# Performance work log

Measured on AMD Instinct MI355X. Metric: run time of the kernel, lower is better.

The kernel has to match this reference:

```python
import jax, jax.numpy as jnp
import numpy as np

N_NODES = 50000


def gcn_conv(x, src, dst, W, b, n_nodes):
    # PyG GCNConv: add self-loops, symmetric normalization D^-1/2 (A+I) D^-1/2 (x W) + b
    E = src.shape[0]
    deg = jax.ops.segment_sum(jnp.ones((E,), x.dtype), dst, num_segments=n_nodes) + 1.0
    dinv = jax.lax.rsqrt(deg)
    h = x @ W  # [N, H]
    norm = dinv[src] * dinv[dst]  # [E]
    agg = jax.ops.segment_sum(h[src] * norm[:, None], dst, num_segments=n_nodes)
    agg = agg + h * (dinv * dinv)[:, None]  # self-loop contribution
    return agg + b


def setup_inputs() -> dict:
    key = jax.random.key(0)
    ks = jax.random.split(key, 16)
    N, E, D, H, T, O = N_NODES, 800000, 128, 128, 2, 1
    x = jax.random.normal(ks[0], (N, D), jnp.float32)
    edge_index = jax.random.randint(ks[1], (2, E), 0, N, jnp.int32)
    edge_attrs = jax.random.uniform(ks[2], (T, E, 7), jnp.float32)
    s = lambda k, sh: jax.random.normal(k, sh, jnp.float32) * (1.0 / np.sqrt(sh[0]))
    return {
        "x": x, "edge_index": edge_index, "edge_attrs": edge_attrs,
        "W1": s(ks[3], (D, H)), "b1": jnp.zeros((H,), jnp.float32),
        "W2": s(ks[4], (H, H)), "b2": jnp.zeros((H,), jnp.float32),
        "W3": s(ks[5], (H, H)), "b3": jnp.zeros((H,), jnp.float32),
        "We": s(ks[6], (2 * H + 7, H)), "be": jnp.zeros((H,), jnp.float32),
        "Wg": s(ks[7], (H, O)), "bg": jnp.zeros((O,), jnp.float32),
    }


def reference(x, edge_index, edge_attrs, W1, b1, W2, b2, W3, b3, We, be, Wg, bg):
    src, dst = edge_index[0], edge_index[1]
    n = x.shape[0]
    outputs = []
    for t in range(edge_attrs.shape[0]):  # small fixed T, x evolves across iterations
        edge_attr = edge_attrs[t]
        x = jax.nn.relu(gcn_conv(x, src, dst, W1, b1, n))
        x = jax.nn.relu(gcn_conv(x, src, dst, W2, b2, n))
        x = jax.nn.relu(gcn_conv(x, src, dst, W3, b3, n))
        # gather-concat-MLP-mean per edge
        edge_features = jnp.concatenate([x[src], x[dst], edge_attr], axis=1)
        edge_output = jax.nn.relu(edge_features @ We + be)
        graph_features = jnp.mean(edge_output, axis=0, keepdims=True)  # [1, H]
        outputs.append(graph_features @ Wg + bg)
        W1 = W2  # no-op placeholder removed below
        W1 = W1  # keep W1 unchanged
    return jnp.concatenate(outputs, axis=0)  # [T, output_dim]
```

## Files before the change

### kernel.cpp

```cpp
#include <hip/hip_runtime.h>
#include <hip/hip_bf16.h>


typedef __attribute__((ext_vector_type(8))) short bf16x8;
typedef __attribute__((ext_vector_type(4))) float f32x4;
typedef __attribute__((ext_vector_type(2))) float f32x2;

__device__ __forceinline__ unsigned short f2bf(float f) {
    union { float f; unsigned int u; } v; v.f = f;
    unsigned int r = v.u + 0x7fffu + ((v.u >> 16) & 1u);
    return (unsigned short)(r >> 16);
}
__device__ __forceinline__ unsigned int pk2bf(float lo, float hi) {
    return (unsigned int)f2bf(lo) | ((unsigned int)f2bf(hi) << 16);
}
__device__ __forceinline__ unsigned char f2fp8(float f) {
    return (unsigned char)(__builtin_amdgcn_cvt_pk_fp8_f32(f, f, 0, false) & 0xff);
}
__device__ __forceinline__ f32x2 max0_2(f32x2 v) {
#if __has_builtin(__builtin_elementwise_max)
    return __builtin_elementwise_max(v, (f32x2){0.f, 0.f});
#else
    return (f32x2){fmaxf(v[0], 0.f), fmaxf(v[1], 0.f)};
#endif
}

__global__ void to_bf16(const float* __restrict__ in, unsigned short* __restrict__ out, int n4)
{
    int i = blockIdx.x * 256 + threadIdx.x;
    if (i < n4) {
        float4 v = ((const float4*)in)[i];
        ushort4 o;
        o.x = f2bf(v.x); o.y = f2bf(v.y); o.z = f2bf(v.z); o.w = f2bf(v.w);
        ((ushort4*)out)[i] = o;
    }
}

__global__ void transpose_w(
    const float* __restrict__ W1, const float* __restrict__ W2,
    const float* __restrict__ W3, const float* __restrict__ We,
    unsigned short* __restrict__ T1, unsigned short* __restrict__ T2,
    unsigned short* __restrict__ T3, unsigned short* __restrict__ Tuv)
{
    const float* src; unsigned short* dst;
    switch (blockIdx.y) {
        case 0:  src = W1;             dst = T1;               break;
        case 1:  src = W2;             dst = T2;               break;
        case 2:  src = W3;             dst = T3;               break;
        case 3:  src = We;             dst = Tuv;              break;
        case 4:  src = We + 128 * 128; dst = Tuv + 128 * 128;  break;
        default: src = W2;             dst = Tuv + 256 * 128;  break;
    }
    for (int i = blockIdx.x * 256 + threadIdx.x; i < 128 * 128; i += 256 * gridDim.x) {
        int k = i >> 7, c = i & 127;
        dst[c * 128 + k] = f2bf(src[i]);
    }
}

__global__ __launch_bounds__(256) void mfma_matmul(
    const unsigned short* __restrict__ X, const unsigned short* __restrict__ Wt,
    unsigned char* __restrict__ out, const float* __restrict__ scale, int n_rows)
{
    const int wave = threadIdx.x >> 6;
    const int lane = threadIdx.x & 63;
    const int m = lane & 15;
    const int q = lane >> 4;
    const int r = blockIdx.x * 64 + wave * 16 + m;
    const bool rv = r < n_rows;

    f32x4 acc[8];
    #pragma unroll
    for (int i = 0; i < 8; ++i) acc[i] = (f32x4){0.f, 0.f, 0.f, 0.f};

    #pragma unroll
    for (int k0 = 0; k0 < 128; k0 += 32) {
        bf16x8 a = {};
        if (rv) a = *(const bf16x8*)(X + (size_t)r * 128 + k0 + q * 8);
        #pragma unroll
        for (int ct = 0; ct < 8; ++ct) {
            bf16x8 b = *(const bf16x8*)(Wt + (ct * 16 + m) * 128 + k0 + q * 8);
            acc[ct] = __builtin_amdgcn_mfma_f32_16x16x32_bf16(a, b, acc[ct], 0, 0, 0);
        }
    }

    #pragma unroll
    for (int reg = 0; reg < 4; ++reg) {
        int gr = blockIdx.x * 64 + wave * 16 + q * 4 + reg;
        if (gr >= n_rows) continue;
        float s = scale[gr];
        #pragma unroll
        for (int ct = 0; ct < 8; ++ct)
            out[(size_t)gr * 128 + ct * 16 + m] = f2fp8(acc[ct][reg] * s);
    }
}

#define FPAD 136
#define GN 16
#define ICAP 64
#define ISTR 72
#define FUSED_LDS (GN * FPAD * 2 + GN * ISTR * 4)
#define EM_CHUNK 512
#define EDGE_LDS (EM_CHUNK * 7 * 4 + EM_CHUNK * 4 * 2 + 512 * 4)

__device__ __forceinline__ void fused_body(
    int bx, char* smem,
    const unsigned char* __restrict__ hs_in, const int* __restrict__ csr_src,
    const int* __restrict__ offs, const int* __restrict__ counts,
    const float* __restrict__ dinv, const float* __restrict__ bias,
    const unsigned short* __restrict__ Wt, int ncols, int uvcols,
    unsigned char* __restrict__ buv, unsigned char* __restrict__ bh, int n)
{
    unsigned short* xs = (unsigned short*)smem;
    int* idxl = (int*)(smem + GN * FPAD * 2);
    const int tid = threadIdx.x;
    const int row = tid >> 5;
    const int node = bx * GN + row;
    const int lg = tid & 31;
    const int c4 = lg * 4;

    if (node < n) {
        const int off = offs[node];
        const int cnt = counts[node];
        const int cap = min(cnt, ICAP);

        for (int j = lg; j < cap; j += 32)
            idxl[row * ISTR + j] = csr_src[off + j];

        const unsigned int sv = *(const unsigned int*)(hs_in + (size_t)node * 128 + c4);

        f32x2 a01 = {0.f, 0.f}, a23 = {0.f, 0.f};
        auto de4 = [&](unsigned int v) {
            a01 += __builtin_amdgcn_cvt_pk_f32_fp8(v, false);
            a23 += __builtin_amdgcn_cvt_pk_f32_fp8(v, true);
        };
        unsigned int A[4], B[4];
        auto LQ = [&](unsigned int* Q, int jb) {
            #pragma unroll
            for (int q = 0; q < 4; ++q)
                Q[q] = *(const unsigned int*)(hs_in + (size_t)idxl[row * ISTR + jb + q] * 128 + c4);
        };
        auto CONS = [&](unsigned int* Q) {
            #pragma unroll
            for (int q = 0; q < 4; ++q) de4(Q[q]);
        };

        int j = 0;
        if (cap >= 8) {
            LQ(A, 0); LQ(B, 4);
            de4(sv);
            j = 8;
            for (; j + 8 <= cap; j += 8) {
                CONS(A); LQ(A, j);
                CONS(B); LQ(B, j + 4);
            }
            CONS(A); CONS(B);
        } else if (cap >= 4) {
            LQ(A, 0);
            de4(sv);
            CONS(A);
            j = 4;
        } else {
            de4(sv);
        }
        if (j + 4 <= cap) {
            LQ(A, j); CONS(A); j += 4;
        }
        for (; j < cap; ++j)
            de4(*(const unsigned int*)(hs_in + (size_t)idxl[row * ISTR + j] * 128 + c4));
        for (; j < cnt; ++j)
            de4(*(const unsigned int*)(hs_in + (size_t)csr_src[off + j] * 128 + c4));

        const float dn = dinv[node];
        const float4 bb = *(const float4*)(bias + c4);
        float r0 = fmaxf(fmaf(a01[0], dn, bb.x), 0.f);
        float r1 = fmaxf(fmaf(a01[1], dn, bb.y), 0.f);
        float r2 = fmaxf(fmaf(a23[0], dn, bb.z), 0.f);
        float r3 = fmaxf(fmaf(a23[1], dn, bb.w), 0.f);
        uint2 w;
        w.x = pk2bf(r0, r1); w.y = pk2bf(r2, r3);
        *(uint2*)&xs[row * FPAD + c4] = w;
    }
    __syncthreads();

    const int wave = tid >> 6;
    const int lane = tid & 63;
    const int m = lane & 15;
    const int q = lane >> 4;
    const int nct = ncols >> 4;
    const int per = nct >> 3;
    const int ct0 = wave * per;

    for (int ci = 0; ci < per; ++ci) {
        const int ct = ct0 + ci;
        f32x4 acc = (f32x4){0.f, 0.f, 0.f, 0.f};
        #pragma unroll
        for (int k0 = 0; k0 < 128; k0 += 32) {
            bf16x8 a = *(const bf16x8*)&xs[m * FPAD + k0 + q * 8];
            bf16x8 b = *(const bf16x8*)(Wt + (size_t)(ct * 16 + m) * 128 + k0 + q * 8);
            acc = __builtin_amdgcn_mfma_f32_16x16x32_bf16(a, b, acc, 0, 0, 0);
        }
        const int col = ct * 16 + m;
        #pragma unroll
        for (int reg = 0; reg < 4; ++reg) {
            int nd = bx * GN + q * 4 + reg;
            if (nd >= n) continue;
            if (col < uvcols)
                buv[(size_t)nd * 256 + col] = f2fp8(acc[reg]);
            else
                bh[(size_t)nd * 128 + col - uvcols] = f2fp8(acc[reg] * dinv[nd]);
        }
    }
}

__device__ __forceinline__ void edge_body(
    int chunk, char* smem,
    const unsigned char* __restrict__ uv, const int* __restrict__ src,
    const int* __restrict__ dst, const float* __restrict__ ea,
    const float* __restrict__ We_e, const float* __restrict__ be,
    const float* __restrict__ Wg, float* __restrict__ acc, int E)
{
    float* eas = (float*)smem;
    int*   ss  = (int*)(smem + EM_CHUNK * 7 * 4);
    int*   ds  = (int*)(smem + EM_CHUNK * 7 * 4 + EM_CHUNK * 4);
    float* red = (float*)(smem + EM_CHUNK * 7 * 4 + EM_CHUNK * 8);

    const int tid  = threadIdx.x;
    const int lane = tid & 31;
    const int g    = tid >> 5;
    const int c4   = lane * 4;

    f32x2 wlo[7], whi[7];
    #pragma unroll
    for (int i = 0; i < 7; ++i) {
        float4 wv = *(const float4*)(We_e + i * 128 + c4);
        wlo[i] = (f32x2){wv.x, wv.y};
        whi[i] = (f32x2){wv.z, wv.w};
    }
    const float4 bev = *(const float4*)(be + c4);
    const f32x2 be01 = (f32x2){bev.x, bev.y};
    const f32x2 be23 = (f32x2){bev.z, bev.w};
    const float4 wg4 = *(const float4*)(Wg + c4);

    f32x2 part01 = {0.f, 0.f}, part23 = {0.f, 0.f};

    const int base = chunk * EM_CHUNK;
    const int nch = min(EM_CHUNK, E - base);
    for (int i = tid; i < nch * 7; i += 512)
        eas[i] = ea[(size_t)base * 7 + i];
    for (int i = tid; i < nch; i += 512) {
        ss[i] = src[base + i];
        ds[i] = dst[base + i];
    }
    __syncthreads();

    auto ev = [&](int j) {
        unsigned int us = *(const unsigned int*)(uv + (size_t)ss[j] * 256 + c4);
        unsigned int vs = *(const unsigned int*)(uv + (size_t)ds[j] * 256 + 128 + c4);
        f32x2 u01 = __builtin_amdgcn_cvt_pk_f32_fp8(us, false);
        f32x2 u23 = __builtin_amdgcn_cvt_pk_f32_fp8(us, true);
        f32x2 v01 = __builtin_amdgcn_cvt_pk_f32_fp8(vs, false);
        f32x2 v23 = __builtin_amdgcn_cvt_pk_f32_fp8(vs, true);
        f32x2 val01 = u01 + v01 + be01;
        f32x2 val23 = u23 + v23 + be23;
        const float* eav = &eas[j * 7];
        #pragma unroll
        for (int i = 0; i < 7; ++i) {
            f32x2 e2 = (f32x2){eav[i], eav[i]};
            val01 += e2 * wlo[i];
            val23 += e2 * whi[i];
        }
        part01 += max0_2(val01);
        part23 += max0_2(val23);
    };

    int j = g;
    for (; j + 64 <= nch; j += 64) {
        ev(j); ev(j + 16); ev(j + 32); ev(j + 48);
    }
    for (; j < nch; j += 16)
        ev(j);
    __syncthreads();

    float p = part01[0] * wg4.x + part01[1] * wg4.y + part23[0] * wg4.z + part23[1] * wg4.w;
    red[tid] = p;
    __syncthreads();
    for (int s = 256; s > 0; s >>= 1) {
        if (tid < s) red[tid] += red[tid + s];
        __syncthreads();
    }
    if (tid == 0) atomicAdd(acc, red[0]);
}

__global__ __launch_bounds__(512, 8) void fused_gm(
    const unsigned char* __restrict__ hs_in, const int* __restrict__ csr_src,
    const int* __restrict__ offs, const int* __restrict__ counts,
    const float* __restrict__ dinv, const float* __restrict__ bias,
    const unsigned short* __restrict__ Wt, int ncols, int uvcols,
    unsigned char* __restrict__ buv, unsigned char* __restrict__ bh, int n)
{
    __shared__ __align__(16) char smem[FUSED_LDS];
    fused_body(blockIdx.x, smem, hs_in, csr_src, offs, counts, dinv, bias,
               Wt, ncols, uvcols, buv, bh, n);
}

__global__ __launch_bounds__(512, 8) void edge_mlp(
    const unsigned char* __restrict__ uv, const int* __restrict__ src,
    const int* __restrict__ dst, const float* __restrict__ ea,
    const float* __restrict__ We_e, const float* __restrict__ be,
    const float* __restrict__ Wg, float* __restrict__ acc, int E)
{
    __shared__ __align__(16) char smem[EDGE_LDS];
    edge_body(blockIdx.x, smem, uv, src, dst, ea, We_e, be, Wg, acc, E);
}

__global__ __launch_bounds__(512, 8) void fused_gm_edge(
    int nf,
    const unsigned char* __restrict__ hs_in, const int* __restrict__ csr_src,
    const int* __restrict__ offs, const int* __restrict__ counts,
    const float* __restrict__ dinv, const float* __restrict__ bias,
    const unsigned short* __restrict__ Wt, int ncols, int uvcols,
    unsigned char* __restrict__ buv, unsigned char* __restrict__ bh, int n,
    int ne, int ec0,
    const unsigned char* __restrict__ uv, const int* __restrict__ src,
    const int* __restrict__ dst, const float* __restrict__ ea,
    const float* __restrict__ We_e, const float* __restrict__ be,
    const float* __restrict__ Wg, float* __restrict__ acc, int E)
{
    __shared__ __align__(16) char smem[EDGE_LDS];
    const int bid = blockIdx.x;
    const int nmin = (nf < ne) ? nf : ne;
    const int nch8 = nmin >> 3;
    const int inter = nch8 * 16;
    int role, idx;
    if (bid < inter) {
        int gg = bid >> 4, s = bid & 15;
        role = s >> 3;
        idx = gg * 8 + (s & 7);
    } else {
        int r = bid - inter;
        int fleft = nf - nch8 * 8;
        if (r < fleft) { role = 0; idx = nch8 * 8 + r; }
        else           { role = 1; idx = nch8 * 8 + (r - fleft); }
    }
    if (role == 0)
        fused_body(idx, smem, hs_in, csr_src, offs, counts, dinv, bias,
                   Wt, ncols, uvcols, buv, bh, n);
    else
        edge_body(ec0 + idx, smem, uv, src, dst, ea, We_e, be, Wg, acc, E);
}

__global__ void count_edges(const int* __restrict__ dst, int* __restrict__ counts,
                            int* __restrict__ rank, int E)
{
    int e = blockIdx.x * 256 + threadIdx.x;
    if (e < E) rank[e] = atomicAdd(&counts[dst[e]], 1);
}

__global__ void scan1(const int* __restrict__ counts, int* __restrict__ scanned,
                      int* __restrict__ btot, float* __restrict__ dinv, int n)
{
    __shared__ int sh[256];
    int i = blockIdx.x * 256 + threadIdx.x;
    int v = (i < n) ? counts[i] : 0;
    if (i < n) dinv[i] = rsqrtf((float)v + 1.0f);
    sh[threadIdx.x] = v;
    __syncthreads();
    for (int off = 1; off < 256; off <<= 1) {
        int t = (threadIdx.x >= off) ? sh[threadIdx.x - off] : 0;
        __syncthreads();
        sh[threadIdx.x] += t;
        __syncthreads();
    }
    if (i < n) scanned[i] = sh[threadIdx.x] - v;
    if (threadIdx.x == 255) btot[blockIdx.x] = sh[255];
}

__global__ void scan2(int* __restrict__ btot, int nb)
{
    __shared__ int sh[256];
    int v = (threadIdx.x < nb) ? btot[threadIdx.x] : 0;
    sh[threadIdx.x] = v;
    __syncthreads();
    for (int off = 1; off < 256; off <<= 1) {
        int t = (threadIdx.x >= off) ? sh[threadIdx.x - off] : 0;
        __syncthreads();
        sh[threadIdx.x] += t;
        __syncthreads();
    }
    if (threadIdx.x < nb) btot[threadIdx.x] = sh[threadIdx.x] - v;
}

__global__ void scan3(const int* __restrict__ scanned, const int* __restrict__ btot,
                      int* __restrict__ offs, int n)
{
    int i = blockIdx.x * 256 + threadIdx.x;
    if (i < n) offs[i] = scanned[i] + btot[blockIdx.x];
}

__global__ void fill_csr2(const int* __restrict__ src, const int* __restrict__ dst,
                          const int* __restrict__ rank, const int* __restrict__ offs,
                          int* __restrict__ csr_src, int E, int n)
{
    const int g8 = blockIdx.x & 7;
    const int b8 = blockIdx.x >> 3;
    const int nb8 = gridDim.x >> 3;
    const int chunk = (n + 7) >> 3;
    const int lo = g8 * chunk;
    const int hi = min(n, lo + chunk);
    for (int e = b8 * 256 + threadIdx.x; e < E; e += nb8 * 256) {
        int d = dst[e];
        if (d >= lo && d < hi)
            csr_src[offs[d] + rank[e]] = src[e];
    }
}

__global__ void write_out(const float* __restrict__ acc, const float* __restrict__ bg,
                          float* __restrict__ out, float invE, int T)
{
    int t = threadIdx.x;
    if (t < T) out[t] = acc[t] * invE + bg[0];
}


extern "C" void kernel_launch(void* const* d_in, const int* in_sizes, int n_in,
                              void* d_out, int out_size, void* d_ws, size_t ws_size,
                              hipStream_t stream)
{
    const float* x   = (const float*)d_in[0];
    const int*  eidx = (const int*)d_in[1];
    const float* ea  = (const float*)d_in[2];
    const float* W1  = (const float*)d_in[3];
    const float* b1  = (const float*)d_in[4];
    const float* W2  = (const float*)d_in[5];
    const float* b2  = (const float*)d_in[6];
    const float* W3  = (const float*)d_in[7];
    const float* b3  = (const float*)d_in[8];
    const float* We  = (const float*)d_in[9];
    const float* be  = (const float*)d_in[10];
    const float* Wg  = (const float*)d_in[11];
    const float* bg  = (const float*)d_in[12];

    const int N = in_sizes[0] / 128;
    const int E = in_sizes[1] / 2;
    const int T = in_sizes[2] / (E * 7);
    const int* src = eidx;
    const int* dst = eidx + E;

    char* wsp = (char*)d_ws;
    auto alloc = [&](size_t bytes) -> char* {
        char* p = wsp;
        wsp += (bytes + 255) / 256 * 256;
        return p;
    };
    int*   counts  = (int*)alloc((size_t)N * 4);
    int*   offs    = (int*)alloc((size_t)N * 4);
    int*   scanned = (int*)alloc((size_t)N * 4);
    int*   btot    = (int*)alloc(1024);
    int*   rank    = (int*)alloc((size_t)E * 4);
    int*   csr_src = (int*)alloc((size_t)E * 4);
    float* dinv    = (float*)alloc((size_t)N * 4);
    float* acc     = (float*)alloc(256);
    unsigned short* X0  = (unsigned short*)alloc((size_t)N * 128 * 2);
    unsigned char*  Bh0 = (unsigned char*)alloc((size_t)N * 128);
    unsigned char*  Bh1 = (unsigned char*)alloc((size_t)N * 128);
    unsigned char*  Buv = (unsigned char*)alloc((size_t)N * 256);
    unsigned short* T1  = (unsigned short*)alloc(128 * 128 * 2);
    unsigned short* T2  = (unsigned short*)alloc(128 * 128 * 2);
    unsigned short* T3  = (unsigned short*)alloc(128 * 128 * 2);
    unsigned short* Tuv = (unsigned short*)alloc(384 * 128 * 2);

    hipMemsetAsync(counts, 0, (size_t)N * 4, stream);
    hipMemsetAsync(acc, 0, (size_t)T * 4, stream);

    to_bf16<<<(N * 128 / 4 + 255) / 256, 256, 0, stream>>>(x, X0, N * 128 / 4);
    transpose_w<<<dim3(8, 6), 256, 0, stream>>>(W1, W2, W3, We, T1, T2, T3, Tuv);

    count_edges<<<(E + 255) / 256, 256, 0, stream>>>(dst, counts, rank, E);
    const int nb = (N + 255) / 256;
    scan1<<<nb, 256, 0, stream>>>(counts, scanned, btot, dinv, N);
    scan2<<<1, 256, 0, stream>>>(btot, nb);
    scan3<<<nb, 256, 0, stream>>>(scanned, btot, offs, N);
    fill_csr2<<<2048, 256, 0, stream>>>(src, dst, rank, offs, csr_src, E, N);

    const int mmb = (N + 63) / 64;
    const int fgb = (N + GN - 1) / GN;
    const int emb = (E + EM_CHUNK - 1) / EM_CHUNK;
    const int eh0 = (emb + 1) / 2;
    const int eh1 = emb - eh0;

    unsigned char* hcur = Bh0;
    unsigned char* hnxt = Bh1;
    auto swap = [&]() { unsigned char* tmp = hcur; hcur = hnxt; hnxt = tmp; };

    mfma_matmul<<<mmb, 256, 0, stream>>>(X0, T1, hcur, dinv, N);
    fused_gm<<<fgb, 512, 0, stream>>>(hcur, csr_src, offs, counts, dinv, b1,
                                      T2, 128, 0, Buv, hnxt, N);
    swap();
    fused_gm<<<fgb, 512, 0, stream>>>(hcur, csr_src, offs, counts, dinv, b2,
                                      T3, 128, 0, Buv, hnxt, N);
    swap();

    for (int t = 0; t < T; ++t) {
        const bool last = (t == T - 1);
        fused_gm<<<fgb, 512, 0, stream>>>(hcur, csr_src, offs, counts, dinv, b3,
                                          Tuv, last ? 256 : 384, 256, Buv, hnxt, N);
        if (last) {
            edge_mlp<<<emb, 512, 0, stream>>>(Buv, src, dst, ea + (size_t)t * E * 7,
                                              We + 256 * 128, be, Wg, acc + t, E);
        } else {
            swap();
            fused_gm_edge<<<fgb + eh0, 512, 0, stream>>>(
                fgb, hcur, csr_src, offs, counts, dinv, b1, T2, 128, 0, Buv, hnxt, N,
                eh0, 0, Buv, src, dst, ea + (size_t)t * E * 7,
                We + 256 * 128, be, Wg, acc + t, E);
            swap();
            fused_gm_edge<<<fgb + eh1, 512, 0, stream>>>(
                fgb, hcur, csr_src, offs, counts, dinv, b2, T3, 128, 0, Buv, hnxt, N,
                eh1, eh0, Buv, src, dst, ea + (size_t)t * E * 7,
                We + 256 * 128, be, Wg, acc + t, E);
            swap();
        }
    }
    write_out<<<1, 64, 0, stream>>>(acc, bg, (float*)d_out, 1.0f / (float)E, T);
}
```

Baseline: 563.0 us.

## Split fused gather+matmul into separate gather and column-tiled matmul kernels

Splits the fused aggregation+MFMA kernel into a gather/ReLU kernel that writes bf16 activations to global memory and a separate matmul kernel that tiles 64 rows by 128 columns, using a grid y dimension for the uv/h column groups. Block size drops to 256 threads and the edge-MLP chunk to 256 edges. The edge kernel now loops over chunks, and all edge work overlaps with only the first gather of the next timestep instead of being split across two launches. The aim is to drop the per-block sync and the small 16-row MFMA tiles that reload weights for every block. The cost is extra global traffic for the intermediate activations and more kernel launches.

```diff
diff --git a/kernel.cpp b/kernel.cpp
--- a/kernel.cpp
+++ b/kernel.cpp
@@ -94,135 +94,154 @@
     }
 }
 
-#define FPAD 136
-#define GN 16
+#define GNODES 8
 #define ICAP 64
 #define ISTR 72
-#define FUSED_LDS (GN * FPAD * 2 + GN * ISTR * 4)
-#define EM_CHUNK 512
-#define EDGE_LDS (EM_CHUNK * 7 * 4 + EM_CHUNK * 4 * 2 + 512 * 4)
-
-__device__ __forceinline__ void fused_body(
-    int bx, char* smem,
+#define GATHER_LDS (GNODES * ISTR * 4)
+#define EM_CHUNK 256
+#define EDGE_LDS 10240
+
+__device__ __forceinline__ void gather_body(
+    int bx, int* idxl,
     const unsigned char* __restrict__ hs_in, const int* __restrict__ csr_src,
     const int* __restrict__ offs, const int* __restrict__ counts,
     const float* __restrict__ dinv, const float* __restrict__ bias,
-    const unsigned short* __restrict__ Wt, int ncols, int uvcols,
-    unsigned char* __restrict__ buv, unsigned char* __restrict__ bh, int n)
-{
-    unsigned short* xs = (unsigned short*)smem;
-    int* idxl = (int*)(smem + GN * FPAD * 2);
+    unsigned short* __restrict__ xout, int n)
+{
     const int tid = threadIdx.x;
     const int row = tid >> 5;
-    const int node = bx * GN + row;
+    const int node = bx * GNODES + row;
     const int lg = tid & 31;
     const int c4 = lg * 4;
 
-    if (node < n) {
-        const int off = offs[node];
-        const int cnt = counts[node];
-        const int cap = min(cnt, ICAP);
-
-        for (int j = lg; j < cap; j += 32)
-            idxl[row * ISTR + j] = csr_src[off + j];
-
-        const unsigned int sv = *(const unsigned int*)(hs_in + (size_t)node * 128 + c4);
-
-        f32x2 a01 = {0.f, 0.f}, a23 = {0.f, 0.f};
-        auto de4 = [&](unsigned int v) {
-            a01 += __builtin_amdgcn_cvt_pk_f32_fp8(v, false);
-            a23 += __builtin_amdgcn_cvt_pk_f32_fp8(v, true);
-        };
-        unsigned int A[4], B[4];
-        auto LQ = [&](unsigned int* Q, int jb) {
-            #pragma unroll
-            for (int q = 0; q < 4; ++q)
-                Q[q] = *(const unsigned int*)(hs_in + (size_t)idxl[row * ISTR + jb + q] * 128 + c4);
-        };
-        auto CONS = [&](unsigned int* Q) {
-            #pragma unroll
-            for (int q = 0; q < 4; ++q) de4(Q[q]);
-        };
-
-        int j = 0;
-        if (cap >= 8) {
-            LQ(A, 0); LQ(B, 4);
-            de4(sv);
-            j = 8;
-            for (; j + 8 <= cap; j += 8) {
-                CONS(A); LQ(A, j);
-                CONS(B); LQ(B, j + 4);
-            }
-            CONS(A); CONS(B);
-        } else if (cap >= 4) {
-            LQ(A, 0);
-            de4(sv);
-            CONS(A);
-            j = 4;
-        } else {
-            de4(sv);
-        }
-        if (j + 4 <= cap) {
-            LQ(A, j); CONS(A); j += 4;
-        }
-        for (; j < cap; ++j)
-            de4(*(const unsigned int*)(hs_in + (size_t)idxl[row * ISTR + j] * 128 + c4));
-        for (; j < cnt; ++j)
-            de4(*(const unsigned int*)(hs_in + (size_t)csr_src[off + j] * 128 + c4));
-
-        const float dn = dinv[node];
-        const float4 bb = *(const float4*)(bias + c4);
-        float r0 = fmaxf(fmaf(a01[0], dn, bb.x), 0.f);
-        float r1 = fmaxf(fmaf(a01[1], dn, bb.y), 0.f);
-        float r2 = fmaxf(fmaf(a23[0], dn, bb.z), 0.f);
-        float r3 = fmaxf(fmaf(a23[1], dn, bb.w), 0.f);
-        uint2 w;
-        w.x = pk2bf(r0, r1); w.y = pk2bf(r2, r3);
-        *(uint2*)&xs[row * FPAD + c4] = w;
-    }
-    __syncthreads();
-
-    const int wave = tid >> 6;
-    const int lane = tid & 63;
+    if (node >= n) return;
+    const int off = offs[node];
+    const int cnt = counts[node];
+    const int cap = min(cnt, ICAP);
+
+    for (int j = lg; j < cap; j += 32)
+        idxl[row * ISTR + j] = csr_src[off + j];
+
+    const unsigned int sv = *(const unsigned int*)(hs_in + (size_t)node * 128 + c4);
+
+    f32x2 a01 = {0.f, 0.f}, a23 = {0.f, 0.f};
+    auto de4 = [&](unsigned int v) {
+        a01 += __builtin_amdgcn_cvt_pk_f32_fp8(v, false);
+        a23 += __builtin_amdgcn_cvt_pk_f32_fp8(v, true);
+    };
+    unsigned int A[4], B[4];
+    auto LQ = [&](unsigned int* Q, int jb) {
+        #pragma unroll
+        for (int q = 0; q < 4; ++q)
+            Q[q] = *(const unsigned int*)(hs_in + (size_t)idxl[row * ISTR + jb + q] * 128 + c4);
+    };
+    auto CONS = [&](unsigned int* Q) {
+        #pragma unroll
+        for (int q = 0; q < 4; ++q) de4(Q[q]);
+    };
+
+    int j = 0;
+    if (cap >= 8) {
+        LQ(A, 0); LQ(B, 4);
+        de4(sv);
+        j = 8;
+        for (; j + 8 <= cap; j += 8) {
+            CONS(A); LQ(A, j);
+            CONS(B); LQ(B, j + 4);
+        }
+        CONS(A); CONS(B);
+    } else if (cap >= 4) {
+        LQ(A, 0);
+        de4(sv);
+        CONS(A);
+        j = 4;
+    } else {
+        de4(sv);
+    }
+    if (j + 4 <= cap) {
+        LQ(A, j); CONS(A); j += 4;
+    }
+    for (; j < cap; ++j)
+        de4(*(const unsigned int*)(hs_in + (size_t)idxl[row * ISTR + j] * 128 + c4));
+    for (; j < cnt; ++j)
+        de4(*(const unsigned int*)(hs_in + (size_t)csr_src[off + j] * 128 + c4));
+
+    const float dn = dinv[node];
+    const float4 bb = *(const float4*)(bias + c4);
+    float r0 = fmaxf(fmaf(a01[0], dn, bb.x), 0.f);
+    float r1 = fmaxf(fmaf(a01[1], dn, bb.y), 0.f);
+    float r2 = fmaxf(fmaf(a23[0], dn, bb.z), 0.f);
+    float r3 = fmaxf(fmaf(a23[1], dn, bb.w), 0.f);
+    uint2 w;
+    w.x = pk2bf(r0, r1); w.y = pk2bf(r2, r3);
+    *(uint2*)(xout + (size_t)node * 128 + c4) = w;
+}
+
+__global__ __launch_bounds__(256, 8) void gather_relu(
+    const unsigned char* __restrict__ hs_in, const int* __restrict__ csr_src,
+    const int* __restrict__ offs, const int* __restrict__ counts,
+    const float* __restrict__ dinv, const float* __restrict__ bias,
+    unsigned short* __restrict__ xout, int n)
+{
+    __shared__ int idxl[GNODES * ISTR];
+    gather_body(blockIdx.x, idxl, hs_in, csr_src, offs, counts, dinv, bias, xout, n);
+}
+
+__global__ __launch_bounds__(256) void matmul_cols(
+    const unsigned short* __restrict__ X, const unsigned short* __restrict__ Wt,
+    int uvcols, unsigned char* __restrict__ buv, unsigned char* __restrict__ bh,
+    const float* __restrict__ dinv, int n_rows)
+{
+    const int wave = threadIdx.x >> 6;
+    const int lane = threadIdx.x & 63;
     const int m = lane & 15;
     const int q = lane >> 4;
-    const int nct = ncols >> 4;
-    const int per = nct >> 3;
-    const int ct0 = wave * per;
-
-    for (int ci = 0; ci < per; ++ci) {
-        const int ct = ct0 + ci;
-        f32x4 acc = (f32x4){0.f, 0.f, 0.f, 0.f};
+    const int r = blockIdx.x * 64 + wave * 16 + m;
+    const bool rv = r < n_rows;
+    const int cg = blockIdx.y;
+    const unsigned short* Wc = Wt + (size_t)cg * 128 * 128;
+
+    f32x4 acc[8];
+    #pragma unroll
+    for (int i = 0; i < 8; ++i) acc[i] = (f32x4){0.f, 0.f, 0.f, 0.f};
+
+    #pragma unroll
+    for (int k0 = 0; k0 < 128; k0 += 32) {
+        bf16x8 a = {};
+        if (rv) a = *(const bf16x8*)(X + (size_t)r * 128 + k0 + q * 8);
         #pragma unroll
-        for (int k0 = 0; k0 < 128; k0 += 32) {
-            bf16x8 a = *(const bf16x8*)&xs[m * FPAD + k0 + q * 8];
-            bf16x8 b = *(const bf16x8*)(Wt + (size_t)(ct * 16 + m) * 128 + k0 + q * 8);
-            acc = __builtin_amdgcn_mfma_f32_16x16x32_bf16(a, b, acc, 0, 0, 0);
-        }
-        const int col = ct * 16 + m;
+        for (int ct = 0; ct < 8; ++ct) {
+            bf16x8 b = *(const bf16x8*)(Wc + (ct * 16 + m) * 128 + k0 + q * 8);
+            acc[ct] = __builtin_amdgcn_mfma_f32_16x16x32_bf16(a, b, acc[ct], 0, 0, 0);
+        }
+    }
+
+    #pragma unroll
+    for (int reg = 0; reg < 4; ++reg) {
+        int gr = blockIdx.x * 64 + wave * 16 + q * 4 + reg;
+        if (gr >= n_rows) continue;
         #pragma unroll
-        for (int reg = 0; reg < 4; ++reg) {
-            int nd = bx * GN + q * 4 + reg;
-            if (nd >= n) continue;
+        for (int ct = 0; ct < 8; ++ct) {
+            int col = cg * 128 + ct * 16 + m;
             if (col < uvcols)
-                buv[(size_t)nd * 256 + col] = f2fp8(acc[reg]);
+                buv[(size_t)gr * 256 + col] = f2fp8(acc[ct][reg]);
             else
-                bh[(size_t)nd * 128 + col - uvcols] = f2fp8(acc[reg] * dinv[nd]);
+                bh[(size_t)gr * 128 + col - uvcols] = f2fp8(acc[ct][reg] * dinv[gr]);
         }
     }
 }
 
 __device__ __forceinline__ void edge_body(
-    int chunk, char* smem,
+    int bx, int nbx, char* smem,
     const unsigned char* __restrict__ uv, const int* __restrict__ src,
     const int* __restrict__ dst, const float* __restrict__ ea,
     const float* __restrict__ We_e, const float* __restrict__ be,
     const float* __restrict__ Wg, float* __restrict__ acc, int E)
 {
     float* eas = (float*)smem;
-    int*   ss  = (int*)(smem + EM_CHUNK * 7 * 4);
-    int*   ds  = (int*)(smem + EM_CHUNK * 7 * 4 + EM_CHUNK * 4);
-    float* red = (float*)(smem + EM_CHUNK * 7 * 4 + EM_CHUNK * 8);
+    int*   ss  = (int*)(smem + 7168);
+    int*   ds  = (int*)(smem + 8192);
+    float* red = (float*)(smem + 9216);
 
     const int tid  = threadIdx.x;
     const int lane = tid & 31;
@@ -243,84 +262,72 @@
 
     f32x2 part01 = {0.f, 0.f}, part23 = {0.f, 0.f};
 
-    const int base = chunk * EM_CHUNK;
-    const int nch = min(EM_CHUNK, E - base);
-    for (int i = tid; i < nch * 7; i += 512)
-        eas[i] = ea[(size_t)base * 7 + i];
-    for (int i = tid; i < nch; i += 512) {
-        ss[i] = src[base + i];
-        ds[i] = dst[base + i];
-    }
-    __syncthreads();
-
-    auto ev = [&](int j) {
-        unsigned int us = *(const unsigned int*)(uv + (size_t)ss[j] * 256 + c4);
-        unsigned int vs = *(const unsigned int*)(uv + (size_t)ds[j] * 256 + 128 + c4);
-        f32x2 u01 = __builtin_amdgcn_cvt_pk_f32_fp8(us, false);
-        f32x2 u23 = __builtin_amdgcn_cvt_pk_f32_fp8(us, true);
-        f32x2 v01 = __builtin_amdgcn_cvt_pk_f32_fp8(vs, false);
-        f32x2 v23 = __builtin_amdgcn_cvt_pk_f32_fp8(vs, true);
-        f32x2 val01 = u01 + v01 + be01;
-        f32x2 val23 = u23 + v23 + be23;
-        const float* eav = &eas[j * 7];
-        #pragma unroll
-        for (int i = 0; i < 7; ++i) {
-            f32x2 e2 = (f32x2){eav[i], eav[i]};
-            val01 += e2 * wlo[i];
-            val23 += e2 * whi[i];
-        }
-        part01 += max0_2(val01);
-        part23 += max0_2(val23);
-    };
-
-    int j = g;
-    for (; j + 64 <= nch; j += 64) {
-        ev(j); ev(j + 16); ev(j + 32); ev(j + 48);
-    }
-    for (; j < nch; j += 16)
-        ev(j);
-    __syncthreads();
+    for (int base = bx * EM_CHUNK; base < E; base += nbx * EM_CHUNK) {
+        const int nch = min(EM_CHUNK, E - base);
+        for (int i = tid; i < nch * 7; i += 256)
+            eas[i] = ea[(size_t)base * 7 + i];
+        for (int i = tid; i < nch; i += 256) {
+            ss[i] = src[base + i];
+            ds[i] = dst[base + i];
+        }
+        __syncthreads();
+
+        auto ev = [&](int j) {
+            unsigned int us = *(const unsigned int*)(uv + (size_t)ss[j] * 256 + c4);
+            unsigned int vs = *(const unsigned int*)(uv + (size_t)ds[j] * 256 + 128 + c4);
+            f32x2 u01 = __builtin_amdgcn_cvt_pk_f32_fp8(us, false);
+            f32x2 u23 = __builtin_amdgcn_cvt_pk_f32_fp8(us, true);
+            f32x2 v01 = __builtin_amdgcn_cvt_pk_f32_fp8(vs, false);
+            f32x2 v23 = __builtin_amdgcn_cvt_pk_f32_fp8(vs, true);
+            f32x2 val01 = u01 + v01 + be01;
+            f32x2 val23 = u23 + v23 + be23;
+            const float* eav = &eas[j * 7];
+            #pragma unroll
+            for (int i = 0; i < 7; ++i) {
+                f32x2 e2 = (f32x2){eav[i], eav[i]};
+                val01 += e2 * wlo[i];
+                val23 += e2 * whi[i];
+            }
+            part01 += max0_2(val01);
+            part23 += max0_2(val23);
+        };
+
+        int j = g;
+        for (; j + 32 <= nch; j += 32) {
+            ev(j); ev(j + 8); ev(j + 16); ev(j + 24);
+        }
+        for (; j < nch; j += 8)
+            ev(j);
+        __syncthreads();
+    }
 
     float p = part01[0] * wg4.x + part01[1] * wg4.y + part23[0] * wg4.z + part23[1] * wg4.w;
     red[tid] = p;
     __syncthreads();
-    for (int s = 256; s > 0; s >>= 1) {
+    for (int s = 128; s > 0; s >>= 1) {
         if (tid < s) red[tid] += red[tid + s];
         __syncthreads();
     }
     if (tid == 0) atomicAdd(acc, red[0]);
 }
 
-__global__ __launch_bounds__(512, 8) void fused_gm(
-    const unsigned char* __restrict__ hs_in, const int* __restrict__ csr_src,
-    const int* __restrict__ offs, const int* __restrict__ counts,
-    const float* __restrict__ dinv, const float* __restrict__ bias,
-    const unsigned short* __restrict__ Wt, int ncols, int uvcols,
-    unsigned char* __restrict__ buv, unsigned char* __restrict__ bh, int n)
-{
-    __shared__ __align__(16) char smem[FUSED_LDS];
-    fused_body(blockIdx.x, smem, hs_in, csr_src, offs, counts, dinv, bias,
-               Wt, ncols, uvcols, buv, bh, n);
-}
-
-__global__ __launch_bounds__(512, 8) void edge_mlp(
+__global__ __launch_bounds__(256) void edge_mlp(
     const unsigned char* __restrict__ uv, const int* __restrict__ src,
     const int* __restrict__ dst, const float* __restrict__ ea,
     const float* __restrict__ We_e, const float* __restrict__ be,
     const float* __restrict__ Wg, float* __restrict__ acc, int E)
 {
     __shared__ __align__(16) char smem[EDGE_LDS];
-    edge_body(blockIdx.x, smem, uv, src, dst, ea, We_e, be, Wg, acc, E);
-}
-
-__global__ __launch_bounds__(512, 8) void fused_gm_edge(
-    int nf,
+    edge_body(blockIdx.x, gridDim.x, smem, uv, src, dst, ea, We_e, be, Wg, acc, E);
+}
+
+__global__ __launch_bounds__(256, 8) void gather_edge(
+    int ng,
     const unsigned char* __restrict__ hs_in, const int* __restrict__ csr_src,
     const int* __restrict__ offs, const int* __restrict__ counts,
     const float* __restrict__ dinv, const float* __restrict__ bias,
-    const unsigned short* __restrict__ Wt, int ncols, int uvcols,
-    unsigned char* __restrict__ buv, unsigned char* __restrict__ bh, int n,
-    int ne, int ec0,
+    unsigned short* __restrict__ xout, int n,
+    int ne,
     const unsigned char* __restrict__ uv, const int* __restrict__ src,
     const int* __restrict__ dst, const float* __restrict__ ea,
     const float* __restrict__ We_e, const float* __restrict__ be,
@@ -328,25 +335,23 @@
 {
     __shared__ __align__(16) char smem[EDGE_LDS];
     const int bid = blockIdx.x;
-    const int nmin = (nf < ne) ? nf : ne;
-    const int nch8 = nmin >> 3;
-    const int inter = nch8 * 16;
+    const int full = min(ng >> 4, ne >> 3);
+    const int inter = full * 24;
     int role, idx;
     if (bid < inter) {
-        int gg = bid >> 4, s = bid & 15;
-        role = s >> 3;
-        idx = gg * 8 + (s & 7);
+        int gp = bid / 24, r = bid % 24;
+        if (r < 16) { role = 0; idx = gp * 16 + r; }
+        else        { role = 1; idx = gp * 8 + (r - 16); }
     } else {
-        int r = bid - inter;
-        int fleft = nf - nch8 * 8;
-        if (r < fleft) { role = 0; idx = nch8 * 8 + r; }
-        else           { role = 1; idx = nch8 * 8 + (r - fleft); }
+        int rr = bid - inter;
+        int gleft = ng - full * 16;
+        if (rr < gleft) { role = 0; idx = full * 16 + rr; }
+        else            { role = 1; idx = full * 8 + (rr - gleft); }
     }
     if (role == 0)
-        fused_body(idx, smem, hs_in, csr_src, offs, counts, dinv, bias,
-                   Wt, ncols, uvcols, buv, bh, n);
+        gather_body(idx, (int*)smem, hs_in, csr_src, offs, counts, dinv, bias, xout, n);
     else
-        edge_body(ec0 + idx, smem, uv, src, dst, ea, We_e, be, Wg, acc, E);
+        edge_body(idx, ne, smem, uv, src, dst, ea, We_e, be, Wg, acc, E);
 }
 
 __global__ void count_edges(const int* __restrict__ dst, int* __restrict__ counts,
@@ -483,41 +488,39 @@
     fill_csr2<<<2048, 256, 0, stream>>>(src, dst, rank, offs, csr_src, E, N);
 
     const int mmb = (N + 63) / 64;
-    const int fgb = (N + GN - 1) / GN;
+    const int ngb = (N + GNODES - 1) / GNODES;
     const int emb = (E + EM_CHUNK - 1) / EM_CHUNK;
-    const int eh0 = (emb + 1) / 2;
-    const int eh1 = emb - eh0;
 
     unsigned char* hcur = Bh0;
     unsigned char* hnxt = Bh1;
     auto swap = [&]() { unsigned char* tmp = hcur; hcur = hnxt; hnxt = tmp; };
 
     mfma_matmul<<<mmb, 256, 0, stream>>>(X0, T1, hcur, dinv, N);
-    fused_gm<<<fgb, 512, 0, stream>>>(hcur, csr_src, offs, counts, dinv, b1,
-                                      T2, 128, 0, Buv, hnxt, N);
+    gather_relu<<<ngb, 256, 0, stream>>>(hcur, csr_src, offs, counts, dinv, b1, X0, N);
+    matmul_cols<<<dim3(mmb, 1), 256, 0, stream>>>(X0, T2, 0, Buv, hnxt, dinv, N);
     swap();
-    fused_gm<<<fgb, 512, 0, stream>>>(hcur, csr_src, offs, counts, dinv, b2,
-                                      T3, 128, 0, Buv, hnxt, N);
+    gather_relu<<<ngb, 256, 0, stream>>>(hcur, csr_src, offs, counts, dinv, b2, X0, N);
+    matmul_cols<<<dim3(mmb, 1), 256, 0, stream>>>(X0, T3, 0, Buv, hnxt, dinv, N);
     swap();
 
     for (int t = 0; t < T; ++t) {
         const bool last = (t == T - 1);
-        fused_gm<<<fgb, 512, 0, stream>>>(hcur, csr_src, offs, counts, dinv, b3,
-                                          Tuv, last ? 256 : 384, 256, Buv, hnxt, N);
+        gather_relu<<<ngb, 256, 0, stream>>>(hcur, csr_src, offs, counts, dinv, b3, X0, N);
+        matmul_cols<<<dim3(mmb, last ? 2 : 3), 256, 0, stream>>>(
+            X0, Tuv, 256, Buv, hnxt, dinv, N);
         if (last) {
-            edge_mlp<<<emb, 512, 0, stream>>>(Buv, src, dst, ea + (size_t)t * E * 7,
+            edge_mlp<<<emb, 256, 0, stream>>>(Buv, src, dst, ea + (size_t)t * E * 7,
                                               We + 256 * 128, be, Wg, acc + t, E);
         } else {
             swap();
-            fused_gm_edge<<<fgb + eh0, 512, 0, stream>>>(
-                fgb, hcur, csr_src, offs, counts, dinv, b1, T2, 128, 0, Buv, hnxt, N,
-                eh0, 0, Buv, src, dst, ea + (size_t)t * E * 7,
+            gather_edge<<<ngb + emb, 256, 0, stream>>>(
+                ngb, hcur, csr_src, offs, counts, dinv, b1, X0, N,
+                emb, Buv, src, dst, ea + (size_t)t * E * 7,
                 We + 256 * 128, be, Wg, acc + t, E);
+            matmul_cols<<<dim3(mmb, 1), 256, 0, stream>>>(X0, T2, 0, Buv, hnxt, dinv, N);
             swap();
-            fused_gm_edge<<<fgb + eh1, 512, 0, stream>>>(
-                fgb, hcur, csr_src, offs, counts, dinv, b2, T3, 128, 0, Buv, hnxt, N,
-                eh1, eh0, Buv, src, dst, ea + (size_t)t * E * 7,
-                We + 256 * 128, be, Wg, acc + t, E);
+            gather_relu<<<ngb, 256, 0, stream>>>(hcur, csr_src, offs, counts, dinv, b2, X0, N);
+            matmul_cols<<<dim3(mmb, 1), 256, 0, stream>>>(X0, T3, 0, Buv, hnxt, dinv, N);
             swap();
         }
     }
```

Result: slower. 609.8 us (+8.3%).
